# Optimization experiments

Measured on AMD Instinct MI355X. Metric: run time of the kernel, lower is better.

## Reference

```python
import jax, jax.numpy as jnp
import numpy as np

D_MODEL = 1024

def setup_inputs() -> dict:
    key = jax.random.key(0)
    ks = jax.random.split(key, 8)
    B, S, D = 8, 2048, D_MODEL
    scale = 1.0 / np.sqrt(D)
    return {
        "x1": jax.random.normal(ks[0], (B, S, D), dtype=jnp.float32),
        "x2": jax.random.normal(ks[1], (B, S, D), dtype=jnp.float32),
        "Wq": jax.random.normal(ks[2], (D, D), dtype=jnp.float32) * scale,
        "bq": jnp.zeros((D,), dtype=jnp.float32),
        "Wk": jax.random.normal(ks[3], (D, D), dtype=jnp.float32) * scale,
        "bk": jnp.zeros((D,), dtype=jnp.float32),
        "Wv": jax.random.normal(ks[4], (D, D), dtype=jnp.float32) * scale,
        "bv": jnp.zeros((D,), dtype=jnp.float32),
    }

def reference(x1, x2, Wq, bq, Wk, bk, Wv, bv):
    # q1: [B, Sq, D]; k2, v2: [B, Sk, D]
    q1 = jnp.einsum('bsd,de->bse', x1, Wq) + bq
    k2 = jnp.einsum('bsd,de->bse', x2, Wk) + bk
    v2 = jnp.einsum('bsd,de->bse', x2, Wv) + bv
    scale = 1.0 / np.sqrt(q1.shape[-1]).astype(np.float32)
    scores = jnp.einsum('bqd,bkd->bqk', q1, k2) * scale  # [B, Sq, Sk]
    probs = jax.nn.softmax(scores, axis=-1)
    return jnp.einsum('bqk,bkd->bqd', probs, v2)
```

## Files before the change

kernel.cpp:

```cpp
#include <hip/hip_runtime.h>
#include <hip/hip_bf16.h>
#include <hip/hip_fp16.h>

typedef __attribute__((ext_vector_type(8))) short short8;
typedef __attribute__((ext_vector_type(4))) float f32x4;

#define DEVI __device__ __forceinline__

DEVI unsigned short f2bf(float f){
  __hip_bfloat16 h = __float2bfloat16(f);
  unsigned short u; __builtin_memcpy(&u, &h, 2); return u;
}

__global__ void cast_f32_bf16(const float* __restrict__ in, unsigned short* __restrict__ out, int n4){
  int stride = gridDim.x * blockDim.x;
  for (int i = blockIdx.x*blockDim.x + threadIdx.x; i < n4; i += stride){
    float4 f = reinterpret_cast<const float4*>(in)[i];
    ushort4 o;
    o.x = f2bf(f.x); o.y = f2bf(f.y); o.z = f2bf(f.z); o.w = f2bf(f.w);
    reinterpret_cast<ushort4*>(out)[i] = o;
  }
}

__global__ void transpose_cast_w(const float* __restrict__ W, unsigned short* __restrict__ WT, int K, int N){
  __shared__ float tile[32][33];
  int bn = blockIdx.x*32, bk = blockIdx.y*32;
  int tx = threadIdx.x & 31, ty = threadIdx.x >> 5;
  for (int r=0;r<32;r+=8)
    tile[ty+r][tx] = W[(long)(bk+ty+r)*N + bn+tx];
  __syncthreads();
  for (int r=0;r<32;r+=8)
    WT[(long)(bn+ty+r)*K + bk+tx] = (short)f2bf(tile[tx][ty+r]);
}

DEVI void stage16(const short* gsrc, short* lbase){
  __builtin_amdgcn_global_load_lds(
      (const __attribute__((address_space(1))) unsigned int*)gsrc,
      (__attribute__((address_space(3))) unsigned int*)lbase, 16, 0, 0);
}

DEVI void stage2(const short* base, long o0, long o1, short* blk, int w){
  stage16(base + o0, blk + w*512);
  stage16(base + o1, blk + (8+w)*512);
}

template<int OT, int BIAS>
__global__ __launch_bounds__(512, 2)
void gemm8(const short* __restrict__ A, const short* __restrict__ Bt,
           const float* __restrict__ bias, void* __restrict__ Cv,
           int N, int K, long sA, long sB, long sC, float scale, int nx, int ny)
{
  extern __shared__ short lds[];
  const int nwg = gridDim.x;
  const int cpx = nwg >> 3;
  const int wg  = (blockIdx.x & 7)*cpx + (blockIdx.x >> 3);
  const int bx  = wg % nx;
  const int tmp = wg / nx;
  const int by  = tmp % ny;
  const long bz = tmp / ny;
  const int m0 = bx * 256, n0 = by * 256;
  const short* Ab = A  + bz*sA + (long)m0 * K;
  const short* Bb = Bt + bz*sB + (long)n0 * K;

  const int t = threadIdx.x, lane = t & 63, w = t >> 6;
  const int wr = w >> 2, wc = w & 3;

  const int rr = lane >> 2;
  const int kk = ((lane & 3) * 8) ^ ((lane & 32) ? 16 : 0);
  const long off0 = (long)(( w     )*16 + rr) * K + kk;
  const long off1 = (long)(( 8 + w )*16 + rr) * K + kk;

  const int la = lane & 15;
  const int lsw = (la*64 + ((lane>>4)<<4)) ^ ((la>=8)?32:0);
  const short* AP = lds + (lsw>>1) + wr*4096;
  const short* BP = lds + (lsw>>1) + 16384 + wc*2048;

  f32x4 acc[8][4] = {};
  short8 bv[4];

  const int NT = K >> 6;
  const int niter = NT >> 1;

  stage2(Ab,      off0, off1, lds + 0,     w);
  stage2(Bb,      off0, off1, lds + 16384, w);
  stage2(Ab + 32, off0, off1, lds + 8192,  w);
  stage2(Bb + 32, off0, off1, lds + 24576, w);
  stage2(Ab + 64, off0, off1, lds + 32768, w);
  stage2(Bb + 64, off0, off1, lds + 49152, w);
  asm volatile("s_waitcnt vmcnt(4)" ::: "memory");
  asm volatile("s_barrier" ::: "memory");

#define PH(CBUF, QM, QK, SBASE, SOFF, SBLK, TAILVM) do {                        \
    const short* ap_ = AP + (CBUF)*32768 + (QK)*8192 + (QM)*2048;               \
    short8 a0_ = *reinterpret_cast<const short8*>(ap_ + 0*512);                 \
    short8 a1_ = *reinterpret_cast<const short8*>(ap_ + 1*512);                 \
    short8 a2_ = *reinterpret_cast<const short8*>(ap_ + 2*512);                 \
    short8 a3_ = *reinterpret_cast<const short8*>(ap_ + 3*512);                 \
    if ((QM) == 0){                                                             \
      const short* bp_ = BP + (CBUF)*32768 + (QK)*8192;                         \
      bv[0] = *reinterpret_cast<const short8*>(bp_ + 0*512);                    \
      bv[1] = *reinterpret_cast<const short8*>(bp_ + 1*512);                    \
      bv[2] = *reinterpret_cast<const short8*>(bp_ + 2*512);                    \
      bv[3] = *reinterpret_cast<const short8*>(bp_ + 3*512);                    \
    }                                                                           \
    stage2((SBASE) + (SOFF), off0, off1, lds + (SBLK), w);                      \
    asm volatile("s_barrier" ::: "memory");                                     \
    asm volatile("s_waitcnt lgkmcnt(0)" ::: "memory");                          \
    __builtin_amdgcn_s_setprio(1);                                              \
    { short8 av_[4] = {a0_, a1_, a2_, a3_};                                     \
      _Pragma("unroll")                                                         \
      for (int i_=0;i_<4;i_++){                                                 \
        _Pragma("unroll")                                                       \
        for (int j_=0;j_<4;j_++)                                                \
          acc[(QM)*4+i_][j_] = __builtin_amdgcn_mfma_f32_16x16x32_bf16(         \
              av_[i_], bv[j_], acc[(QM)*4+i_][j_], 0, 0, 0);                    \
      }                                                                         \
    }                                                                           \
    __builtin_amdgcn_s_setprio(0);                                              \
    if (TAILVM) asm volatile("s_waitcnt vmcnt(4)" ::: "memory");                \
    asm volatile("s_barrier" ::: "memory");                                     \
  } while(0)

  for (int it = 0; it < niter; ++it){
    const int u  = it*2;
    int u1 = u+1; if (u1 >= NT) u1 -= NT;
    int u2 = u+2; if (u2 >= NT) u2 -= NT;
    int u3 = u+3; if (u3 >= NT) u3 -= NT;
    const int k1 = u1*64, k2 = u2*64, k3 = u3*64;
    PH(0, 0, 0, Ab, k1+32, 40960, 0);
    PH(0, 1, 0, Bb, k1+32, 57344, 0);
    PH(0, 0, 1, Ab, k2,    0,     0);
    PH(0, 1, 1, Bb, k2,    16384, 1);
    PH(1, 0, 0, Ab, k2+32, 8192,  0);
    PH(1, 1, 0, Bb, k2+32, 24576, 0);
    PH(1, 0, 1, Ab, k3,    32768, 0);
    PH(1, 1, 1, Bb, k3,    49152, 1);
  }
#undef PH

  {
    char* sb = (char*)lds;
    constexpr int STRB = (OT==0) ? 1056 : 544;
    const int tr = t >> 4, tcE = (t & 15) * 16;
    const int grow = m0 + (tr>>4)*128 + (tr&15);
    #pragma unroll
    for (int mi = 0; mi < 8; ++mi){
      __syncthreads();
      #pragma unroll
      for (int nj = 0; nj < 4; ++nj){
        const int c = wc*64 + la + nj*16;
        float badd = (BIAS==1) ? bias[n0 + c] : 0.0f;
        #pragma unroll
        for (int j = 0; j < 4; ++j){
          const int lr = wr*16 + ((lane>>4)<<2) + j;
          float v = acc[mi][nj][j] * scale + badd;
          if (BIAS==2) v += bias[m0 + (lr>>4)*128 + mi*16 + (lr&15)];
          if constexpr (OT==0){
            const int byte = lr*STRB + ((((c>>2) ^ (lr&15)))<<4) + (c&3)*4;
            *reinterpret_cast<float*>(sb + byte) = v;
          } else if constexpr (OT==1){
            const int byte = lr*STRB + ((((c>>3) ^ (lr&15)))<<4) + (c&7)*2;
            *reinterpret_cast<__half*>(sb + byte) = __float2half(v);
          } else {
            const int byte = lr*STRB + ((((c>>3) ^ (lr&15)))<<4) + (c&7)*2;
            *reinterpret_cast<unsigned short*>(sb + byte) = f2bf(v);
          }
        }
      }
      __syncthreads();
      const long gbase = bz*sC + (long)(grow + mi*16)*N + n0 + tcE;
      if constexpr (OT==0){
        const int cb = tcE >> 2;
        #pragma unroll
        for (int i=0;i<4;i++){
          f32x4 vv = *reinterpret_cast<const f32x4*>(sb + tr*STRB + (((cb+i)^(tr&15))<<4));
          *reinterpret_cast<f32x4*>((float*)Cv + gbase + i*4) = vv;
        }
      } else {
        const int cb = tcE >> 3;
        #pragma unroll
        for (int i=0;i<2;i++){
          short8 vv = *reinterpret_cast<const short8*>(sb + tr*STRB + (((cb+i)^(tr&15))<<4));
          *reinterpret_cast<short8*>((unsigned short*)Cv + gbase + i*8) = vv;
        }
      }
    }
  }
}

__global__ void softmax_rows(unsigned short* __restrict__ SP, int cols){
  const long row = blockIdx.x;
  unsigned short* rp = SP + row * cols;
  const int t = threadIdx.x, lane = t & 63, w = t >> 6;
  short8 raw = *reinterpret_cast<const short8*>(rp + t*8);
  float v[8];
  #pragma unroll
  for (int i=0;i<8;i++){
    unsigned short us = (unsigned short)raw[i];
    __half h; __builtin_memcpy(&h, &us, 2);
    v[i] = __half2float(h);
  }
  float m = v[0];
  #pragma unroll
  for (int i=1;i<8;i++) m = fmaxf(m, v[i]);
  #pragma unroll
  for (int o=32;o;o>>=1) m = fmaxf(m, __shfl_down(m, o));
  __shared__ float red[8];
  if (lane==0) red[w] = m;
  __syncthreads();
  if (t==0) red[4] = fmaxf(fmaxf(red[0],red[1]), fmaxf(red[2],red[3]));
  __syncthreads();
  const float rowmax = red[4];
  float s = 0.f;
  #pragma unroll
  for (int i=0;i<8;i++){ v[i] = __expf(v[i]-rowmax); s += v[i]; }
  #pragma unroll
  for (int o=32;o;o>>=1) s += __shfl_down(s, o);
  if (lane==0) red[w] = s;
  __syncthreads();
  if (t==0) red[5] = red[0]+red[1]+red[2]+red[3];
  __syncthreads();
  const float inv = 1.0f / red[5];
  short8 outp;
  #pragma unroll
  for (int i=0;i<8;i++) outp[i] = (short)f2bf(v[i]*inv);
  *reinterpret_cast<short8*>(rp + t*8) = outp;
}

extern "C" void kernel_launch(void* const* d_in, const int* in_sizes, int n_in,
                              void* d_out, int out_size, void* d_ws, size_t ws_size,
                              hipStream_t stream)
{
  const int B = 8, S = 2048, D = 1024;
  const int BS = B * S;
  const float* x1 = (const float*)d_in[0];
  const float* x2 = (const float*)d_in[1];
  const float* Wq = (const float*)d_in[2];
  const float* bq = (const float*)d_in[3];
  const float* Wk = (const float*)d_in[4];
  const float* bk = (const float*)d_in[5];
  const float* Wv = (const float*)d_in[6];
  const float* bv = (const float*)d_in[7];

  char* ws = (char*)d_ws;
  const size_t MB = 1024*1024;
  short*          x1b = (short*)(ws);
  short*          x2b = (short*)(ws + 32*MB);
  unsigned short* Sc  = (unsigned short*)ws;
  short*          q   = (short*)(ws + 64*MB);
  short*          k   = (short*)(ws + 96*MB);
  short*          vT  = (short*)(ws + 128*MB);
  short*          WqT = (short*)(ws + 160*MB);
  short*          WkT = (short*)(ws + 162*MB);
  short*          WvT = (short*)(ws + 164*MB);

  const size_t SH = 131072;

  cast_f32_bf16<<<4096,256,0,stream>>>(x1, (unsigned short*)x1b, BS*D/4);
  cast_f32_bf16<<<4096,256,0,stream>>>(x2, (unsigned short*)x2b, BS*D/4);
  transpose_cast_w<<<dim3(32,32),256,0,stream>>>(Wq, (unsigned short*)WqT, D, D);
  transpose_cast_w<<<dim3(32,32),256,0,stream>>>(Wk, (unsigned short*)WkT, D, D);
  transpose_cast_w<<<dim3(32,32),256,0,stream>>>(Wv, (unsigned short*)WvT, D, D);

  gemm8<2,1><<<256, 512, SH, stream>>>(x2b, WkT, bk, k, D, D, 0,0,0, 1.0f, 64, 4);
  gemm8<2,2><<<256, 512, SH, stream>>>(WvT, x2b, bv, vT, S, D, 0, (long)S*D, (long)D*S, 1.0f, 4, 8);
  gemm8<2,1><<<256, 512, SH, stream>>>(x1b, WqT, bq, q, D, D, 0,0,0, 1.0f, 64, 4);
  gemm8<1,0><<<512, 512, SH, stream>>>(q, k, nullptr, Sc, S, D,
                                       (long)S*D, (long)S*D, (long)S*S, 0.03125f, 8, 8);
  softmax_rows<<<BS,256,0,stream>>>(Sc, S);
  gemm8<0,0><<<256, 512, SH, stream>>>((short*)Sc, vT, nullptr, d_out, D, S,
                                       (long)S*S, (long)D*S, (long)S*D, 1.0f, 8, 4);
}
```

Measured before the change: 346.5 us.

## Reorder GEMM LDS staging pipeline and split kernels per GEMM role

Restructures the GEMM main loop so B tiles are staged ahead of A, keeps one more staged load in flight (vmcnt 6 instead of 4), and reorders phases to iterate K-halves within each buffer. Adds a partial lgkmcnt wait plus sched_barrier so the compiler cannot move the MFMA block ahead of the LDS reads. Wraps the body in separate named kernels with explicit waves-per-EU attributes, adds a full drain before the epilogue, and reorders the launches so the x1/Wq casts sit next to the Q projection. The goal is to hide global-to-LDS latency more deeply. The cost is tighter buffer-reuse ordering, which risks races if any wait count is wrong.

```diff
diff --git a/kernel.cpp b/kernel.cpp
--- a/kernel.cpp
+++ b/kernel.cpp
@@ -45,10 +45,9 @@
 }
 
 template<int OT, int BIAS>
-__global__ __launch_bounds__(512, 2)
-void gemm8(const short* __restrict__ A, const short* __restrict__ Bt,
-           const float* __restrict__ bias, void* __restrict__ Cv,
-           int N, int K, long sA, long sB, long sC, float scale, int nx, int ny)
+DEVI void gemm8_body(const short* __restrict__ A, const short* __restrict__ Bt,
+                     const float* __restrict__ bias, void* __restrict__ Cv,
+                     int N, int K, long sA, long sB, long sC, float scale, int nx, int ny)
 {
   extern __shared__ short lds[];
   const int nwg = gridDim.x;
@@ -76,48 +75,62 @@
   const short* BP = lds + (lsw>>1) + 16384 + wc*2048;
 
   f32x4 acc[8][4] = {};
-  short8 bv[4];
+  short8 b0,b1,b2,b3;
 
   const int NT = K >> 6;
   const int niter = NT >> 1;
 
+  stage2(Bb,      off0, off1, lds + 16384, w);
   stage2(Ab,      off0, off1, lds + 0,     w);
-  stage2(Bb,      off0, off1, lds + 16384, w);
+  stage2(Bb + 32, off0, off1, lds + 24576, w);
   stage2(Ab + 32, off0, off1, lds + 8192,  w);
-  stage2(Bb + 32, off0, off1, lds + 24576, w);
+  stage2(Bb + 64, off0, off1, lds + 49152, w);
   stage2(Ab + 64, off0, off1, lds + 32768, w);
-  stage2(Bb + 64, off0, off1, lds + 49152, w);
-  asm volatile("s_waitcnt vmcnt(4)" ::: "memory");
+  stage2(Bb + 96, off0, off1, lds + 57344, w);
+  asm volatile("s_waitcnt vmcnt(6)" ::: "memory");
   asm volatile("s_barrier" ::: "memory");
 
-#define PH(CBUF, QM, QK, SBASE, SOFF, SBLK, TAILVM) do {                        \
-    const short* ap_ = AP + (CBUF)*32768 + (QK)*8192 + (QM)*2048;               \
-    short8 a0_ = *reinterpret_cast<const short8*>(ap_ + 0*512);                 \
-    short8 a1_ = *reinterpret_cast<const short8*>(ap_ + 1*512);                 \
-    short8 a2_ = *reinterpret_cast<const short8*>(ap_ + 2*512);                 \
-    short8 a3_ = *reinterpret_cast<const short8*>(ap_ + 3*512);                 \
+#define MM16(QM) \
+    acc[(QM)*4+0][0] = __builtin_amdgcn_mfma_f32_16x16x32_bf16(a0, b0, acc[(QM)*4+0][0],0,0,0); \
+    acc[(QM)*4+0][1] = __builtin_amdgcn_mfma_f32_16x16x32_bf16(a0, b1, acc[(QM)*4+0][1],0,0,0); \
+    acc[(QM)*4+0][2] = __builtin_amdgcn_mfma_f32_16x16x32_bf16(a0, b2, acc[(QM)*4+0][2],0,0,0); \
+    acc[(QM)*4+0][3] = __builtin_amdgcn_mfma_f32_16x16x32_bf16(a0, b3, acc[(QM)*4+0][3],0,0,0); \
+    acc[(QM)*4+1][0] = __builtin_amdgcn_mfma_f32_16x16x32_bf16(a1, b0, acc[(QM)*4+1][0],0,0,0); \
+    acc[(QM)*4+1][1] = __builtin_amdgcn_mfma_f32_16x16x32_bf16(a1, b1, acc[(QM)*4+1][1],0,0,0); \
+    acc[(QM)*4+1][2] = __builtin_amdgcn_mfma_f32_16x16x32_bf16(a1, b2, acc[(QM)*4+1][2],0,0,0); \
+    acc[(QM)*4+1][3] = __builtin_amdgcn_mfma_f32_16x16x32_bf16(a1, b3, acc[(QM)*4+1][3],0,0,0); \
+    acc[(QM)*4+2][0] = __builtin_amdgcn_mfma_f32_16x16x32_bf16(a2, b0, acc[(QM)*4+2][0],0,0,0); \
+    acc[(QM)*4+2][1] = __builtin_amdgcn_mfma_f32_16x16x32_bf16(a2, b1, acc[(QM)*4+2][1],0,0,0); \
+    acc[(QM)*4+2][2] = __builtin_amdgcn_mfma_f32_16x16x32_bf16(a2, b2, acc[(QM)*4+2][2],0,0,0); \
+    acc[(QM)*4+2][3] = __builtin_amdgcn_mfma_f32_16x16x32_bf16(a2, b3, acc[(QM)*4+2][3],0,0,0); \
+    acc[(QM)*4+3][0] = __builtin_amdgcn_mfma_f32_16x16x32_bf16(a3, b0, acc[(QM)*4+3][0],0,0,0); \
+    acc[(QM)*4+3][1] = __builtin_amdgcn_mfma_f32_16x16x32_bf16(a3, b1, acc[(QM)*4+3][1],0,0,0); \
+    acc[(QM)*4+3][2] = __builtin_amdgcn_mfma_f32_16x16x32_bf16(a3, b2, acc[(QM)*4+3][2],0,0,0); \
+    acc[(QM)*4+3][3] = __builtin_amdgcn_mfma_f32_16x16x32_bf16(a3, b3, acc[(QM)*4+3][3],0,0,0);
+
+#define PHASE(BUF, KH, QM, SBASE, SKOFF, SLDS, TAILVM) do {                     \
+    short8 a0,a1,a2,a3;                                                         \
+    const short* ap_ = AP + (BUF)*32768 + (KH)*8192 + (QM)*2048;                \
     if ((QM) == 0){                                                             \
-      const short* bp_ = BP + (CBUF)*32768 + (QK)*8192;                         \
-      bv[0] = *reinterpret_cast<const short8*>(bp_ + 0*512);                    \
-      bv[1] = *reinterpret_cast<const short8*>(bp_ + 1*512);                    \
-      bv[2] = *reinterpret_cast<const short8*>(bp_ + 2*512);                    \
-      bv[3] = *reinterpret_cast<const short8*>(bp_ + 3*512);                    \
+      const short* bp_ = BP + (BUF)*32768 + (KH)*8192;                          \
+      b0 = *reinterpret_cast<const short8*>(bp_ + 0*512);                       \
+      b1 = *reinterpret_cast<const short8*>(bp_ + 1*512);                       \
+      b2 = *reinterpret_cast<const short8*>(bp_ + 2*512);                       \
+      b3 = *reinterpret_cast<const short8*>(bp_ + 3*512);                       \
     }                                                                           \
-    stage2((SBASE) + (SOFF), off0, off1, lds + (SBLK), w);                      \
+    a0 = *reinterpret_cast<const short8*>(ap_ + 0*512);                         \
+    a1 = *reinterpret_cast<const short8*>(ap_ + 1*512);                         \
+    a2 = *reinterpret_cast<const short8*>(ap_ + 2*512);                         \
+    a3 = *reinterpret_cast<const short8*>(ap_ + 3*512);                         \
+    stage2((SBASE) + (SKOFF), off0, off1, lds + (SLDS), w);                     \
+    if ((QM) == 0) asm volatile("s_waitcnt lgkmcnt(4)" ::: "memory");           \
     asm volatile("s_barrier" ::: "memory");                                     \
     asm volatile("s_waitcnt lgkmcnt(0)" ::: "memory");                          \
+    __builtin_amdgcn_sched_barrier(0);                                          \
     __builtin_amdgcn_s_setprio(1);                                              \
-    { short8 av_[4] = {a0_, a1_, a2_, a3_};                                     \
-      _Pragma("unroll")                                                         \
-      for (int i_=0;i_<4;i_++){                                                 \
-        _Pragma("unroll")                                                       \
-        for (int j_=0;j_<4;j_++)                                                \
-          acc[(QM)*4+i_][j_] = __builtin_amdgcn_mfma_f32_16x16x32_bf16(         \
-              av_[i_], bv[j_], acc[(QM)*4+i_][j_], 0, 0, 0);                    \
-      }                                                                         \
-    }                                                                           \
+    MM16(QM)                                                                    \
     __builtin_amdgcn_s_setprio(0);                                              \
-    if (TAILVM) asm volatile("s_waitcnt vmcnt(4)" ::: "memory");                \
+    if (TAILVM) asm volatile("s_waitcnt vmcnt(6)" ::: "memory");                \
     asm volatile("s_barrier" ::: "memory");                                     \
   } while(0)
 
@@ -127,16 +140,20 @@
     int u2 = u+2; if (u2 >= NT) u2 -= NT;
     int u3 = u+3; if (u3 >= NT) u3 -= NT;
     const int k1 = u1*64, k2 = u2*64, k3 = u3*64;
-    PH(0, 0, 0, Ab, k1+32, 40960, 0);
-    PH(0, 1, 0, Bb, k1+32, 57344, 0);
-    PH(0, 0, 1, Ab, k2,    0,     0);
-    PH(0, 1, 1, Bb, k2,    16384, 1);
-    PH(1, 0, 0, Ab, k2+32, 8192,  0);
-    PH(1, 1, 0, Bb, k2+32, 24576, 0);
-    PH(1, 0, 1, Ab, k3,    32768, 0);
-    PH(1, 1, 1, Bb, k3,    49152, 1);
+    PHASE(0,0,0, Ab, k1+32, 40960, 0);
+    PHASE(0,0,1, Bb, k2,    16384, 0);
+    PHASE(0,1,0, Ab, k2,    0,     0);
+    PHASE(0,1,1, Bb, k2+32, 24576, 1);
+    PHASE(1,0,0, Ab, k2+32, 8192,  0);
+    PHASE(1,0,1, Bb, k3,    49152, 0);
+    PHASE(1,1,0, Ab, k3,    32768, 0);
+    PHASE(1,1,1, Bb, k3+32, 57344, 1);
   }
-#undef PH
+#undef PHASE
+#undef MM16
+
+  asm volatile("s_waitcnt vmcnt(0) lgkmcnt(0)" ::: "memory");
+  __syncthreads();
 
   {
     char* sb = (char*)lds;
@@ -188,6 +205,23 @@
   }
 }
 
+#define GATTR __global__ __attribute__((amdgpu_flat_work_group_size(512,512), amdgpu_waves_per_eu(2,2)))
+GATTR void g_proj_k(const short* A, const short* Bt, const float* bias, void* Cv,
+                    int N, int K, long sA, long sB, long sC, float scale, int nx, int ny)
+{ gemm8_body<2,1>(A,Bt,bias,Cv,N,K,sA,sB,sC,scale,nx,ny); }
+GATTR void g_proj_v(const short* A, const short* Bt, const float* bias, void* Cv,
+                    int N, int K, long sA, long sB, long sC, float scale, int nx, int ny)
+{ gemm8_body<2,2>(A,Bt,bias,Cv,N,K,sA,sB,sC,scale,nx,ny); }
+GATTR void g_proj_q(const short* A, const short* Bt, const float* bias, void* Cv,
+                    int N, int K, long sA, long sB, long sC, float scale, int nx, int ny)
+{ gemm8_body<2,1>(A,Bt,bias,Cv,N,K,sA,sB,sC,scale,nx,ny); }
+GATTR void g_score(const short* A, const short* Bt, const float* bias, void* Cv,
+                   int N, int K, long sA, long sB, long sC, float scale, int nx, int ny)
+{ gemm8_body<1,0>(A,Bt,bias,Cv,N,K,sA,sB,sC,scale,nx,ny); }
+GATTR void g_pv(const short* A, const short* Bt, const float* bias, void* Cv,
+                int N, int K, long sA, long sB, long sC, float scale, int nx, int ny)
+{ gemm8_body<0,0>(A,Bt,bias,Cv,N,K,sA,sB,sC,scale,nx,ny); }
+
 __global__ void softmax_rows(unsigned short* __restrict__ SP, int cols){
   const long row = blockIdx.x;
   unsigned short* rp = SP + row * cols;
@@ -256,18 +290,17 @@
 
   const size_t SH = 131072;
 
-  cast_f32_bf16<<<4096,256,0,stream>>>(x1, (unsigned short*)x1b, BS*D/4);
   cast_f32_bf16<<<4096,256,0,stream>>>(x2, (unsigned short*)x2b, BS*D/4);
-  transpose_cast_w<<<dim3(32,32),256,0,stream>>>(Wq, (unsigned short*)WqT, D, D);
   transpose_cast_w<<<dim3(32,32),256,0,stream>>>(Wk, (unsigned short*)WkT, D, D);
   transpose_cast_w<<<dim3(32,32),256,0,stream>>>(Wv, (unsigned short*)WvT, D, D);
-
-  gemm8<2,1><<<256, 512, SH, stream>>>(x2b, WkT, bk, k, D, D, 0,0,0, 1.0f, 64, 4);
-  gemm8<2,2><<<256, 512, SH, stream>>>(WvT, x2b, bv, vT, S, D, 0, (long)S*D, (long)D*S, 1.0f, 4, 8);
-  gemm8<2,1><<<256, 512, SH, stream>>>(x1b, WqT, bq, q, D, D, 0,0,0, 1.0f, 64, 4);
-  gemm8<1,0><<<512, 512, SH, stream>>>(q, k, nullptr, Sc, S, D,
-                                       (long)S*D, (long)S*D, (long)S*S, 0.03125f, 8, 8);
+  g_proj_k<<<256, 512, SH, stream>>>(x2b, WkT, bk, k, D, D, 0,0,0, 1.0f, 64, 4);
+  g_proj_v<<<256, 512, SH, stream>>>(WvT, x2b, bv, vT, S, D, 0, (long)S*D, (long)D*S, 1.0f, 4, 8);
+  cast_f32_bf16<<<4096,256,0,stream>>>(x1, (unsigned short*)x1b, BS*D/4);
+  transpose_cast_w<<<dim3(32,32),256,0,stream>>>(Wq, (unsigned short*)WqT, D, D);
+  g_proj_q<<<256, 512, SH, stream>>>(x1b, WqT, bq, q, D, D, 0,0,0, 1.0f, 64, 4);
+  g_score<<<512, 512, SH, stream>>>(q, k, nullptr, Sc, S, D,
+                                    (long)S*D, (long)S*D, (long)S*S, 0.03125f, 8, 8);
   softmax_rows<<<BS,256,0,stream>>>(Sc, S);
-  gemm8<0,0><<<256, 512, SH, stream>>>((short*)Sc, vT, nullptr, d_out, D, S,
-                                       (long)S*S, (long)D*S, (long)S*D, 1.0f, 8, 4);
-}
+  g_pv<<<256, 512, SH, stream>>>((short*)Sc, vT, nullptr, d_out, D, S,
+                                 (long)S*S, (long)D*S, (long)S*D, 1.0f, 8, 4);
+}
```

Measured after the change: 347.4 us. No clear change (+0.2%).
